# Kernel tuning notes

Hardware: AMD Instinct MI355X
Metric: run time of the kernel (lower is better)

## Reference

```python
import jax, jax.numpy as jnp
import numpy as np

EPS = 1e-12


def setup_inputs() -> dict:
    key = jax.random.key(0)
    k1, k2, k3, k4 = jax.random.split(key, 4)
    N, H, W, D, K = 64, 32, 32, 512, 64
    x = jax.random.normal(k1, (N, H, W, D), dtype=jnp.float32)
    W_assign = jax.random.normal(k2, (D, K), dtype=jnp.float32) * 0.05  # 1x1 conv kernel
    b_assign = jax.random.normal(k3, (K,), dtype=jnp.float32) * 0.05
    C = jax.random.normal(k4, (D, K), dtype=jnp.float32) * 0.05  # cluster centers
    return {"x": x, "W_assign": W_assign, "b_assign": b_assign, "C": C}


def _l2norm(v, axis):
    return v / jnp.sqrt(jnp.sum(v * v, axis=axis, keepdims=True) + EPS)


def reference(x, W_assign, b_assign, C):
    # 1x1 conv = matmul over channel dim: [N,H,W,D] @ [D,K] -> [N,H,W,K]
    s = jnp.einsum('nhwd,dk->nhwk', x, W_assign) + b_assign
    a = jax.nn.softmax(s, axis=-1)                       # soft assignment over K
    # VLAD: v[n,d,k] = sum_hw a[n,h,w,k] * (x[n,h,w,d] + C[d,k])
    # reformulated as two small contractions (no [N,H,W,D,K] intermediate):
    v = jnp.einsum('nhwd,nhwk->ndk', x, a)               # feature-weighted sums
    a_sum = jnp.sum(a, axis=(1, 2))                      # [N,K]
    v = v + a_sum[:, None, :] * C[None, :, :]            # [N,D,K]
    # intra-normalization: L2 over D per cluster (after transpose to [N,K,D])
    v = _l2norm(jnp.transpose(v, (0, 2, 1)), axis=-1)    # [N,K,D]
    v = jnp.transpose(v, (0, 2, 1))                      # [N,D,K]
    # flatten and final L2 normalize -> [N, D*K]
    v = v.reshape(v.shape[0], -1)
    return _l2norm(v, axis=-1)
```

## Files before the change

### kernel.cpp

```cpp
#include <hip/hip_runtime.h>


#define EPSF 1e-12f

typedef short bf16x8 __attribute__((ext_vector_type(8)));
typedef float f32x16 __attribute__((ext_vector_type(16)));

__device__ inline unsigned short f2bf_rne(float f) {
  union { float f; unsigned u; } v; v.f = f;
  unsigned u = v.u;
  unsigned r = u + 0x7fffu + ((u >> 16) & 1u);
  return (unsigned short)(r >> 16);
}
__device__ inline unsigned pk2(float a, float b) {
#if __has_builtin(__builtin_amdgcn_cvt_pk_bf16_f32)
  auto r = __builtin_amdgcn_cvt_pk_bf16_f32(a, b);
  return __builtin_bit_cast(unsigned, r);
#else
  return (unsigned)f2bf_rne(a) | ((unsigned)f2bf_rne(b) << 16);
#endif
}

__global__ __launch_bounds__(256) void kprep(
    const float* __restrict__ Wm, unsigned short* __restrict__ wt,
    float* __restrict__ stats ) {
  const int t = threadIdx.x, bx = blockIdx.x;
  if (bx == 8) {
    float4 z = {0.f, 0.f, 0.f, 0.f};
#pragma unroll
    for (int r = 0; r < 8; ++r)
      *(float4*)&stats[(size_t)(r * 256 + t) * 4] = z;
    return;
  }
  __shared__ float tile[64][65];
  {
    int col = (t & 15) * 4, rbase = t >> 4;
#pragma unroll
    for (int r = 0; r < 4; ++r) {
      int row = rbase + 16 * r;
      *(float4*)&tile[row][col] =
          *(const float4*)&Wm[(size_t)(bx * 64 + row) * 64 + col];
    }
  }
  __syncthreads();
  int k = t >> 2, seg = (t & 3) * 16;
  size_t o = (size_t)k * 512 + bx * 64 + seg;
#pragma unroll
  for (int j = 0; j < 16; j += 2)
    *(unsigned*)&wt[o + j] = pk2(tile[seg + j][k], tile[seg + j + 1][k]);
}

__global__ __launch_bounds__(256, 1) void kfused(
    const float* __restrict__ x, const unsigned short* __restrict__ wt,
    const float* __restrict__ b, float* __restrict__ vpart,
    float* __restrict__ a_sum) {
  __shared__ unsigned short xbT[512 * 128];
  __shared__ unsigned short ab[64 * 128];
  const int t = threadIdx.x;
  const int w = t >> 6, lane = t & 63, l31 = lane & 31, h = lane >> 5;
  const int bid = blockIdx.x;
  const int n = bid >> 2, c = bid & 3;
  const unsigned short* w0 = wt + (size_t)l31 * 512;
  const unsigned short* w1 = wt + (size_t)(32 + l31) * 512;
  const int colpx = w * 32 + l31;

  float bias0[16], bias1[16];
#pragma unroll
  for (int r = 0; r < 16; ++r) {
    const int k0 = (r & 3) + 8 * (r >> 2) + 4 * h;
    bias0[r] = b[k0];
    bias1[r] = b[k0 + 32];
  }

  f32x16 accv[8];
#pragma unroll
  for (int i = 0; i < 8; ++i)
#pragma unroll
    for (int j = 0; j < 16; ++j) accv[i][j] = 0.f;

  float sa0[16], sa1[16];
#pragma unroll
  for (int r = 0; r < 16; ++r) { sa0[r] = 0.f; sa1[r] = 0.f; }

  for (int s = 0; s < 2; ++s) {
    const int pxb = c * 256 + s * 128;
    const float* rowp = x + ((size_t)n * 1024 + pxb + colpx) * 512;
    f32x16 s0, s1;
#pragma unroll
    for (int i = 0; i < 16; ++i) { s0[i] = 0.f; s1[i] = 0.f; }
#pragma unroll 8
    for (int st = 0; st < 32; ++st) {
      const int kd = st * 16 + h * 8;
      float4 xa = *(const float4*)&rowp[kd];
      float4 xb = *(const float4*)&rowp[kd + 4];
      union { unsigned u[4]; bf16x8 v; } ax;
      ax.u[0] = pk2(xa.x, xa.y);
      ax.u[1] = pk2(xa.z, xa.w);
      ax.u[2] = pk2(xb.x, xb.y);
      ax.u[3] = pk2(xb.z, xb.w);
      bf16x8 b0 = *(const bf16x8*)&w0[kd];
      bf16x8 b1 = *(const bf16x8*)&w1[kd];
      s0 = __builtin_amdgcn_mfma_f32_32x32x16_bf16(b0, ax.v, s0, 0, 0, 0);
      s1 = __builtin_amdgcn_mfma_f32_32x32x16_bf16(b1, ax.v, s1, 0, 0, 0);
#pragma unroll
      for (int j2 = 0; j2 < 4; ++j2) {
        const int da = kd + 2 * j2, db = da + 1;
        xbT[da * 128 + (colpx ^ ((da & 15) << 3))] =
            (unsigned short)(ax.u[j2] & 0xffffu);
        xbT[db * 128 + (colpx ^ ((db & 15) << 3))] =
            (unsigned short)(ax.u[j2] >> 16);
      }
    }
    float v0[16], v1[16];
    float m = -3.402823466e+38f;
#pragma unroll
    for (int r = 0; r < 16; ++r) {
      v0[r] = s0[r] + bias0[r];
      v1[r] = s1[r] + bias1[r];
      m = fmaxf(m, fmaxf(v0[r], v1[r]));
    }
    m = fmaxf(m, __shfl_xor(m, 32, 64));
    float e0[16], e1[16];
    float S = 0.f;
#pragma unroll
    for (int r = 0; r < 16; ++r) {
      e0[r] = __expf(v0[r] - m);
      e1[r] = __expf(v1[r] - m);
      S += e0[r] + e1[r];
    }
    S += __shfl_xor(S, 32, 64);
    const float inv = 1.0f / S;
#pragma unroll
    for (int r = 0; r < 16; ++r) {
      const float a0 = e0[r] * inv, a1 = e1[r] * inv;
      sa0[r] += a0; sa1[r] += a1;
      const int k0 = (r & 3) + 8 * (r >> 2) + 4 * h, k1 = k0 + 32;
      ab[k0 * 128 + (colpx ^ ((k0 & 15) << 3))] = f2bf_rne(a0);
      ab[k1 * 128 + (colpx ^ ((k1 & 15) << 3))] = f2bf_rne(a1);
    }
    __syncthreads();
    const int dw = w * 128;
#pragma unroll
    for (int s8 = 0; s8 < 8; ++s8) {
      const int px0 = s8 * 16 + 8 * h;
      bf16x8 bb0 = *(const bf16x8*)&ab[l31 * 128 + (px0 ^ ((l31 & 15) << 3))];
      bf16x8 bb1 =
          *(const bf16x8*)&ab[(32 + l31) * 128 + (px0 ^ ((l31 & 15) << 3))];
#pragma unroll
      for (int dt = 0; dt < 4; ++dt) {
        const int dr = dw + dt * 32 + l31;
        bf16x8 aa = *(const bf16x8*)&xbT[dr * 128 + (px0 ^ ((dr & 15) << 3))];
        accv[dt * 2 + 0] =
            __builtin_amdgcn_mfma_f32_32x32x16_bf16(aa, bb0, accv[dt * 2 + 0], 0, 0, 0);
        accv[dt * 2 + 1] =
            __builtin_amdgcn_mfma_f32_32x32x16_bf16(aa, bb1, accv[dt * 2 + 1], 0, 0, 0);
      }
    }
    __syncthreads();
  }
#pragma unroll
  for (int msk = 1; msk < 32; msk <<= 1) {
#pragma unroll
    for (int r = 0; r < 16; ++r) {
      sa0[r] += __shfl_xor(sa0[r], msk, 64);
      sa1[r] += __shfl_xor(sa1[r], msk, 64);
    }
  }
  if (l31 < 16) {
    const int r = l31;
    const int k0 = (r & 3) + 8 * (r >> 2) + 4 * h;
    atomicAdd(&a_sum[n * 64 + k0], sa0[r]);
    atomicAdd(&a_sum[n * 64 + k0 + 32], sa1[r]);
  }
  float* vp = vpart + (size_t)c * 2097152 + (size_t)n * 32768;
#pragma unroll
  for (int dt = 0; dt < 4; ++dt) {
#pragma unroll
    for (int kt = 0; kt < 2; ++kt) {
      const f32x16 a = accv[dt * 2 + kt];
      const int kcol = kt * 32 + l31;
#pragma unroll
      for (int r = 0; r < 16; ++r) {
        const int drow = w * 128 + dt * 32 + (r & 3) + 8 * (r >> 2) + 4 * h;
        vp[drow * 64 + kcol] = a[r];
      }
    }
  }
}

__global__ __launch_bounds__(256) void kpost(
    const float* __restrict__ vpart, const float* __restrict__ a_sum,
    const float* __restrict__ C, float* __restrict__ out,
    float* __restrict__ ssq) {
  const int bid = blockIdx.x;
  const int n = bid & 63, d0 = (bid >> 6) * 64;
  const int t = threadIdx.x, k = t & 63, dr = t >> 6;
  const float as = a_sum[n * 64 + k];
  const size_t nb = (size_t)n * 32768;
  float sq = 0.f;
#pragma unroll
  for (int r = 0; r < 16; ++r) {
    const int d = d0 + dr * 16 + r;
    const size_t idx = nb + (size_t)d * 64 + k;
    float o = vpart[idx] + vpart[idx + 2097152] + vpart[idx + 4194304] +
              vpart[idx + 6291456] + as * C[(size_t)d * 64 + k];
    out[idx] = o;
    sq += o * o;
  }
  atomicAdd(&ssq[n * 64 + k], sq);
}

__global__ __launch_bounds__(256) void kscale(
    float* __restrict__ out, const float* __restrict__ ssq) {
  const int n = blockIdx.y, slice = blockIdx.x;
  const int t = threadIdx.x, k = t & 63, rg = t >> 6;
  __shared__ float sk[64];
  __shared__ float tot;
  if (t < 64) {
    float cc = ssq[n * 64 + t];
    sk[t] = rsqrtf(cc + EPSF);
    float contrib = cc / (cc + EPSF);
#pragma unroll
    for (int m = 32; m; m >>= 1) contrib += __shfl_xor(contrib, m, 64);
    if (t == 0) tot = rsqrtf(contrib + EPSF);
  }
  __syncthreads();
  const float scale = sk[k] * tot;
  float* vb = out + (size_t)n * 32768 + (size_t)slice * 4096;
#pragma unroll
  for (int r = rg; r < 64; r += 4) vb[r * 64 + k] *= scale;
}

extern "C" void kernel_launch(void* const* d_in, const int* in_sizes, int n_in,
                              void* d_out, int out_size, void* d_ws, size_t ws_size,
                              hipStream_t stream) {
  const float* x  = (const float*)d_in[0];
  const float* Wm = (const float*)d_in[1];
  const float* b  = (const float*)d_in[2];
  const float* C  = (const float*)d_in[3];
  float* out = (float*)d_out;

  float* vpart = (float*)d_ws;
  unsigned short* wt = (unsigned short*)(vpart + (size_t)4 * 2097152);
  float* stats = (float*)(wt + (size_t)64 * 512);
  float* a_sum = stats;
  float* ssq   = stats + 4096;

  kprep<<<dim3(9), dim3(256), 0, stream>>>(Wm, wt, stats);
  kfused<<<dim3(256), dim3(256), 0, stream>>>(x, wt, b, vpart, a_sum);
  kpost<<<dim3(512), dim3(256), 0, stream>>>(vpart, a_sum, C, out, ssq);
  kscale<<<dim3(8, 64), dim3(256), 0, stream>>>(out, ssq);
}
```

Before: 230.1 us.

## Drop LDS x-transpose, re-read x from global, split pixels over 8 blocks

The fused kernel no longer stages a 128 KB bf16 transpose of x in shared memory. Instead the second contraction re-reads x from global memory (likely L2-resident) with strided per-pixel loads and packs it to bf16 in registers. Each block now handles 128 pixels instead of 256, doubling the grid to 512 blocks and allowing more than one block per CU. The cost is a second read of x, strided uncoalesced-ish loads, and twice as many partial VLAD buffers for the post kernel to sum.

```diff
diff --git a/kernel.cpp b/kernel.cpp
--- a/kernel.cpp
+++ b/kernel.cpp
@@ -50,41 +50,21 @@
     *(unsigned*)&wt[o + j] = pk2(tile[seg + j][k], tile[seg + j + 1][k]);
 }
 
-__global__ __launch_bounds__(256, 1) void kfused(
+__global__ __launch_bounds__(256) void kfused(
     const float* __restrict__ x, const unsigned short* __restrict__ wt,
     const float* __restrict__ b, float* __restrict__ vpart,
     float* __restrict__ a_sum) {
-  __shared__ unsigned short xbT[512 * 128];
   __shared__ unsigned short ab[64 * 128];
   const int t = threadIdx.x;
   const int w = t >> 6, lane = t & 63, l31 = lane & 31, h = lane >> 5;
   const int bid = blockIdx.x;
-  const int n = bid >> 2, c = bid & 3;
+  const int n = bid >> 3, c = bid & 7;
   const unsigned short* w0 = wt + (size_t)l31 * 512;
   const unsigned short* w1 = wt + (size_t)(32 + l31) * 512;
   const int colpx = w * 32 + l31;
 
-  float bias0[16], bias1[16];
-#pragma unroll
-  for (int r = 0; r < 16; ++r) {
-    const int k0 = (r & 3) + 8 * (r >> 2) + 4 * h;
-    bias0[r] = b[k0];
-    bias1[r] = b[k0 + 32];
-  }
-
-  f32x16 accv[8];
-#pragma unroll
-  for (int i = 0; i < 8; ++i)
-#pragma unroll
-    for (int j = 0; j < 16; ++j) accv[i][j] = 0.f;
-
-  float sa0[16], sa1[16];
-#pragma unroll
-  for (int r = 0; r < 16; ++r) { sa0[r] = 0.f; sa1[r] = 0.f; }
-
-  for (int s = 0; s < 2; ++s) {
-    const int pxb = c * 256 + s * 128;
-    const float* rowp = x + ((size_t)n * 1024 + pxb + colpx) * 512;
+  {
+    const float* rowp = x + ((size_t)n * 1024 + c * 128 + colpx) * 512;
     f32x16 s0, s1;
 #pragma unroll
     for (int i = 0; i < 16; ++i) { s0[i] = 0.f; s1[i] = 0.f; }
@@ -102,76 +82,84 @@
       bf16x8 b1 = *(const bf16x8*)&w1[kd];
       s0 = __builtin_amdgcn_mfma_f32_32x32x16_bf16(b0, ax.v, s0, 0, 0, 0);
       s1 = __builtin_amdgcn_mfma_f32_32x32x16_bf16(b1, ax.v, s1, 0, 0, 0);
-#pragma unroll
-      for (int j2 = 0; j2 < 4; ++j2) {
-        const int da = kd + 2 * j2, db = da + 1;
-        xbT[da * 128 + (colpx ^ ((da & 15) << 3))] =
-            (unsigned short)(ax.u[j2] & 0xffffu);
-        xbT[db * 128 + (colpx ^ ((db & 15) << 3))] =
-            (unsigned short)(ax.u[j2] >> 16);
-      }
     }
     float v0[16], v1[16];
     float m = -3.402823466e+38f;
 #pragma unroll
     for (int r = 0; r < 16; ++r) {
-      v0[r] = s0[r] + bias0[r];
-      v1[r] = s1[r] + bias1[r];
+      const int k0 = (r & 3) + 8 * (r >> 2) + 4 * h;
+      v0[r] = s0[r] + b[k0];
+      v1[r] = s1[r] + b[k0 + 32];
       m = fmaxf(m, fmaxf(v0[r], v1[r]));
     }
     m = fmaxf(m, __shfl_xor(m, 32, 64));
-    float e0[16], e1[16];
+    float a0[16], a1[16];
     float S = 0.f;
 #pragma unroll
     for (int r = 0; r < 16; ++r) {
-      e0[r] = __expf(v0[r] - m);
-      e1[r] = __expf(v1[r] - m);
-      S += e0[r] + e1[r];
+      a0[r] = __expf(v0[r] - m);
+      a1[r] = __expf(v1[r] - m);
+      S += a0[r] + a1[r];
     }
     S += __shfl_xor(S, 32, 64);
     const float inv = 1.0f / S;
 #pragma unroll
     for (int r = 0; r < 16; ++r) {
-      const float a0 = e0[r] * inv, a1 = e1[r] * inv;
-      sa0[r] += a0; sa1[r] += a1;
+      a0[r] *= inv; a1[r] *= inv;
       const int k0 = (r & 3) + 8 * (r >> 2) + 4 * h, k1 = k0 + 32;
-      ab[k0 * 128 + (colpx ^ ((k0 & 15) << 3))] = f2bf_rne(a0);
-      ab[k1 * 128 + (colpx ^ ((k1 & 15) << 3))] = f2bf_rne(a1);
-    }
-    __syncthreads();
-    const int dw = w * 128;
-#pragma unroll
-    for (int s8 = 0; s8 < 8; ++s8) {
-      const int px0 = s8 * 16 + 8 * h;
-      bf16x8 bb0 = *(const bf16x8*)&ab[l31 * 128 + (px0 ^ ((l31 & 15) << 3))];
-      bf16x8 bb1 =
-          *(const bf16x8*)&ab[(32 + l31) * 128 + (px0 ^ ((l31 & 15) << 3))];
-#pragma unroll
-      for (int dt = 0; dt < 4; ++dt) {
-        const int dr = dw + dt * 32 + l31;
-        bf16x8 aa = *(const bf16x8*)&xbT[dr * 128 + (px0 ^ ((dr & 15) << 3))];
-        accv[dt * 2 + 0] =
-            __builtin_amdgcn_mfma_f32_32x32x16_bf16(aa, bb0, accv[dt * 2 + 0], 0, 0, 0);
-        accv[dt * 2 + 1] =
-            __builtin_amdgcn_mfma_f32_32x32x16_bf16(aa, bb1, accv[dt * 2 + 1], 0, 0, 0);
+      ab[k0 * 128 + (colpx ^ ((k0 & 15) << 3))] = f2bf_rne(a0[r]);
+      ab[k1 * 128 + (colpx ^ ((k1 & 15) << 3))] = f2bf_rne(a1[r]);
+    }
+#pragma unroll
+    for (int msk = 1; msk < 32; msk <<= 1) {
+#pragma unroll
+      for (int r = 0; r < 16; ++r) {
+        a0[r] += __shfl_xor(a0[r], msk, 64);
+        a1[r] += __shfl_xor(a1[r], msk, 64);
       }
     }
-    __syncthreads();
-  }
-#pragma unroll
-  for (int msk = 1; msk < 32; msk <<= 1) {
-#pragma unroll
-    for (int r = 0; r < 16; ++r) {
-      sa0[r] += __shfl_xor(sa0[r], msk, 64);
-      sa1[r] += __shfl_xor(sa1[r], msk, 64);
-    }
-  }
-  if (l31 < 16) {
-    const int r = l31;
-    const int k0 = (r & 3) + 8 * (r >> 2) + 4 * h;
-    atomicAdd(&a_sum[n * 64 + k0], sa0[r]);
-    atomicAdd(&a_sum[n * 64 + k0 + 32], sa1[r]);
-  }
+    if (l31 < 16) {
+      const int r = l31;
+      const int k0 = (r & 3) + 8 * (r >> 2) + 4 * h;
+      atomicAdd(&a_sum[n * 64 + k0], a0[r]);
+      atomicAdd(&a_sum[n * 64 + k0 + 32], a1[r]);
+    }
+  }
+  __syncthreads();
+
+  const int dw = w * 128;
+  f32x16 accv[8];
+#pragma unroll
+  for (int i = 0; i < 8; ++i)
+#pragma unroll
+    for (int j = 0; j < 16; ++j) accv[i][j] = 0.f;
+
+  const float* xg = x + ((size_t)n * 1024 + c * 128) * 512;
+#pragma unroll 2
+  for (int m = 0; m < 8; ++m) {
+    const int px0 = m * 16 + h * 8;
+    bf16x8 bb0 = *(const bf16x8*)&ab[l31 * 128 + (px0 ^ ((l31 & 15) << 3))];
+    bf16x8 bb1 =
+        *(const bf16x8*)&ab[(32 + l31) * 128 + (px0 ^ ((l31 & 15) << 3))];
+#pragma unroll
+    for (int dt = 0; dt < 4; ++dt) {
+      const int d = dw + dt * 32 + l31;
+      const float* xp = xg + (size_t)px0 * 512 + d;
+      float a[8];
+#pragma unroll
+      for (int j = 0; j < 8; ++j) a[j] = xp[(size_t)j * 512];
+      union { unsigned u[4]; bf16x8 v; } aa;
+      aa.u[0] = pk2(a[0], a[1]);
+      aa.u[1] = pk2(a[2], a[3]);
+      aa.u[2] = pk2(a[4], a[5]);
+      aa.u[3] = pk2(a[6], a[7]);
+      accv[dt * 2 + 0] =
+          __builtin_amdgcn_mfma_f32_32x32x16_bf16(aa.v, bb0, accv[dt * 2 + 0], 0, 0, 0);
+      accv[dt * 2 + 1] =
+          __builtin_amdgcn_mfma_f32_32x32x16_bf16(aa.v, bb1, accv[dt * 2 + 1], 0, 0, 0);
+    }
+  }
+
   float* vp = vpart + (size_t)c * 2097152 + (size_t)n * 32768;
 #pragma unroll
   for (int dt = 0; dt < 4; ++dt) {
@@ -181,7 +169,7 @@
       const int kcol = kt * 32 + l31;
 #pragma unroll
       for (int r = 0; r < 16; ++r) {
-        const int drow = w * 128 + dt * 32 + (r & 3) + 8 * (r >> 2) + 4 * h;
+        const int drow = dw + dt * 32 + (r & 3) + 8 * (r >> 2) + 4 * h;
         vp[drow * 64 + kcol] = a[r];
       }
     }
@@ -202,8 +190,9 @@
   for (int r = 0; r < 16; ++r) {
     const int d = d0 + dr * 16 + r;
     const size_t idx = nb + (size_t)d * 64 + k;
-    float o = vpart[idx] + vpart[idx + 2097152] + vpart[idx + 4194304] +
-              vpart[idx + 6291456] + as * C[(size_t)d * 64 + k];
+    float o = as * C[(size_t)d * 64 + k];
+#pragma unroll
+    for (int cc = 0; cc < 8; ++cc) o += vpart[idx + (size_t)cc * 2097152];
     out[idx] = o;
     sq += o * o;
   }
@@ -241,13 +230,13 @@
   float* out = (float*)d_out;
 
   float* vpart = (float*)d_ws;
-  unsigned short* wt = (unsigned short*)(vpart + (size_t)4 * 2097152);
+  unsigned short* wt = (unsigned short*)(vpart + (size_t)8 * 2097152);
   float* stats = (float*)(wt + (size_t)64 * 512);
   float* a_sum = stats;
   float* ssq   = stats + 4096;
 
   kprep<<<dim3(9), dim3(256), 0, stream>>>(Wm, wt, stats);
-  kfused<<<dim3(256), dim3(256), 0, stream>>>(x, wt, b, vpart, a_sum);
+  kfused<<<dim3(512), dim3(256), 0, stream>>>(x, wt, b, vpart, a_sum);
   kpost<<<dim3(512), dim3(256), 0, stream>>>(vpart, a_sum, C, out, ssq);
   kscale<<<dim3(8, 64), dim3(256), 0, stream>>>(out, ssq);
 }
```

New measurement: 254.2 us. 10.5% more time.

## Double-buffer LDS tiles and overlap VLAD MFMA with next chunk's loads

Applied to the files above, without the earlier changes.

Shrinks the per-step pixel chunk from 128 to 64 and splits the channel dimension of the assignment GEMM across wave pairs, reducing partial logits through LDS scratch. LDS tiles for x and assignments are double-buffered so the VLAD accumulation MFMAs for the previous chunk are interleaved with global loads and conversion of the current chunk. This aims to hide global memory latency behind matrix work. It adds extra syncs and an LDS reduction step, and reuses the previous buffer as scratch. Softmax now runs on half the waves.

```diff
diff --git a/kernel.cpp b/kernel.cpp
--- a/kernel.cpp
+++ b/kernel.cpp
@@ -54,123 +54,158 @@
     const float* __restrict__ x, const unsigned short* __restrict__ wt,
     const float* __restrict__ b, float* __restrict__ vpart,
     float* __restrict__ a_sum) {
-  __shared__ unsigned short xbT[512 * 128];
-  __shared__ unsigned short ab[64 * 128];
+  __shared__ unsigned short xbT[2][512 * 64];
+  __shared__ unsigned short ab[2][64 * 64];
   const int t = threadIdx.x;
   const int w = t >> 6, lane = t & 63, l31 = lane & 31, h = lane >> 5;
   const int bid = blockIdx.x;
   const int n = bid >> 2, c = bid & 3;
-  const unsigned short* w0 = wt + (size_t)l31 * 512;
-  const unsigned short* w1 = wt + (size_t)(32 + l31) * 512;
-  const int colpx = w * 32 + l31;
-
-  float bias0[16], bias1[16];
-#pragma unroll
-  for (int r = 0; r < 16; ++r) {
-    const int k0 = (r & 3) + 8 * (r >> 2) + 4 * h;
-    bias0[r] = b[k0];
-    bias1[r] = b[k0 + 32];
-  }
+  const int pxl = (w >> 1) * 32 + l31;
+  const int dhalf = (w & 1) * 256;
+  const unsigned short* wk0 = wt + (size_t)l31 * 512;
+  const unsigned short* wk1 = wt + (size_t)(32 + l31) * 512;
 
   f32x16 accv[8];
 #pragma unroll
   for (int i = 0; i < 8; ++i)
 #pragma unroll
     for (int j = 0; j < 16; ++j) accv[i][j] = 0.f;
-
   float sa0[16], sa1[16];
 #pragma unroll
   for (int r = 0; r < 16; ++r) { sa0[r] = 0.f; sa1[r] = 0.f; }
 
-  for (int s = 0; s < 2; ++s) {
-    const int pxb = c * 256 + s * 128;
-    const float* rowp = x + ((size_t)n * 1024 + pxb + colpx) * 512;
+#pragma unroll
+  for (int s = 0; s < 4; ++s) {
+    const int cur = s & 1, prv = (s + 1) & 1;
+    const float* rowp =
+        x + ((size_t)n * 1024 + c * 256 + s * 64 + pxl) * 512 + dhalf;
     f32x16 s0, s1;
 #pragma unroll
     for (int i = 0; i < 16; ++i) { s0[i] = 0.f; s1[i] = 0.f; }
-#pragma unroll 8
-    for (int st = 0; st < 32; ++st) {
-      const int kd = st * 16 + h * 8;
-      float4 xa = *(const float4*)&rowp[kd];
-      float4 xb = *(const float4*)&rowp[kd + 4];
-      union { unsigned u[4]; bf16x8 v; } ax;
-      ax.u[0] = pk2(xa.x, xa.y);
-      ax.u[1] = pk2(xa.z, xa.w);
-      ax.u[2] = pk2(xb.x, xb.y);
-      ax.u[3] = pk2(xb.z, xb.w);
-      bf16x8 b0 = *(const bf16x8*)&w0[kd];
-      bf16x8 b1 = *(const bf16x8*)&w1[kd];
-      s0 = __builtin_amdgcn_mfma_f32_32x32x16_bf16(b0, ax.v, s0, 0, 0, 0);
-      s1 = __builtin_amdgcn_mfma_f32_32x32x16_bf16(b1, ax.v, s1, 0, 0, 0);
-#pragma unroll
-      for (int j2 = 0; j2 < 4; ++j2) {
-        const int da = kd + 2 * j2, db = da + 1;
-        xbT[da * 128 + (colpx ^ ((da & 15) << 3))] =
-            (unsigned short)(ax.u[j2] & 0xffffu);
-        xbT[db * 128 + (colpx ^ ((db & 15) << 3))] =
-            (unsigned short)(ax.u[j2] >> 16);
-      }
-    }
-    float v0[16], v1[16];
-    float m = -3.402823466e+38f;
-#pragma unroll
-    for (int r = 0; r < 16; ++r) {
-      v0[r] = s0[r] + bias0[r];
-      v1[r] = s1[r] + bias1[r];
-      m = fmaxf(m, fmaxf(v0[r], v1[r]));
-    }
-    m = fmaxf(m, __shfl_xor(m, 32, 64));
-    float e0[16], e1[16];
-    float S = 0.f;
-#pragma unroll
-    for (int r = 0; r < 16; ++r) {
-      e0[r] = __expf(v0[r] - m);
-      e1[r] = __expf(v1[r] - m);
-      S += e0[r] + e1[r];
-    }
-    S += __shfl_xor(S, 32, 64);
-    const float inv = 1.0f / S;
-#pragma unroll
-    for (int r = 0; r < 16; ++r) {
-      const float a0 = e0[r] * inv, a1 = e1[r] * inv;
-      sa0[r] += a0; sa1[r] += a1;
-      const int k0 = (r & 3) + 8 * (r >> 2) + 4 * h, k1 = k0 + 32;
-      ab[k0 * 128 + (colpx ^ ((k0 & 15) << 3))] = f2bf_rne(a0);
-      ab[k1 * 128 + (colpx ^ ((k1 & 15) << 3))] = f2bf_rne(a1);
+
+#pragma unroll
+    for (int u = 0; u < 2; ++u) {
+      float4 xs[16];
+#pragma unroll
+      for (int j = 0; j < 8; ++j) {
+        const int kd = (u * 8 + j) * 16 + h * 8;
+        xs[2 * j]     = *(const float4*)&rowp[kd];
+        xs[2 * j + 1] = *(const float4*)&rowp[kd + 4];
+      }
+      if (s > 0) {
+#pragma unroll
+        for (int ks = 2 * u; ks < 2 * u + 2; ++ks) {
+          const int px0 = ks * 16 + h * 8;
+          bf16x8 bb0 =
+              *(const bf16x8*)&ab[prv][l31 * 64 + (px0 ^ ((l31 & 7) << 3))];
+          bf16x8 bb1 = *(const bf16x8*)&ab[prv][(32 + l31) * 64 +
+                                               (px0 ^ ((l31 & 7) << 3))];
+#pragma unroll
+          for (int dt = 0; dt < 4; ++dt) {
+            const int dr = 128 * w + dt * 32 + l31;
+            bf16x8 aa =
+                *(const bf16x8*)&xbT[prv][dr * 64 + (px0 ^ ((dr & 7) << 3))];
+            accv[dt * 2 + 0] = __builtin_amdgcn_mfma_f32_32x32x16_bf16(
+                aa, bb0, accv[dt * 2 + 0], 0, 0, 0);
+            accv[dt * 2 + 1] = __builtin_amdgcn_mfma_f32_32x32x16_bf16(
+                aa, bb1, accv[dt * 2 + 1], 0, 0, 0);
+          }
+        }
+      }
+#pragma unroll
+      for (int j = 0; j < 8; ++j) {
+        const int kd = (u * 8 + j) * 16 + h * 8;
+        union { unsigned uu[4]; bf16x8 v; } ax;
+        ax.uu[0] = pk2(xs[2 * j].x, xs[2 * j].y);
+        ax.uu[1] = pk2(xs[2 * j].z, xs[2 * j].w);
+        ax.uu[2] = pk2(xs[2 * j + 1].x, xs[2 * j + 1].y);
+        ax.uu[3] = pk2(xs[2 * j + 1].z, xs[2 * j + 1].w);
+#pragma unroll
+        for (int j2 = 0; j2 < 4; ++j2) {
+          const int da = dhalf + kd + 2 * j2, db = da + 1;
+          xbT[cur][da * 64 + (pxl ^ ((da & 7) << 3))] =
+              (unsigned short)(ax.uu[j2] & 0xffffu);
+          xbT[cur][db * 64 + (pxl ^ ((db & 7) << 3))] =
+              (unsigned short)(ax.uu[j2] >> 16);
+        }
+        bf16x8 b0 = *(const bf16x8*)&wk0[dhalf + kd];
+        bf16x8 b1 = *(const bf16x8*)&wk1[dhalf + kd];
+        s0 = __builtin_amdgcn_mfma_f32_32x32x16_bf16(b0, ax.v, s0, 0, 0, 0);
+        s1 = __builtin_amdgcn_mfma_f32_32x32x16_bf16(b1, ax.v, s1, 0, 0, 0);
+      }
     }
     __syncthreads();
-    const int dw = w * 128;
-#pragma unroll
-    for (int s8 = 0; s8 < 8; ++s8) {
-      const int px0 = s8 * 16 + 8 * h;
-      bf16x8 bb0 = *(const bf16x8*)&ab[l31 * 128 + (px0 ^ ((l31 & 15) << 3))];
-      bf16x8 bb1 =
-          *(const bf16x8*)&ab[(32 + l31) * 128 + (px0 ^ ((l31 & 15) << 3))];
-#pragma unroll
-      for (int dt = 0; dt < 4; ++dt) {
-        const int dr = dw + dt * 32 + l31;
-        bf16x8 aa = *(const bf16x8*)&xbT[dr * 128 + (px0 ^ ((dr & 15) << 3))];
-        accv[dt * 2 + 0] =
-            __builtin_amdgcn_mfma_f32_32x32x16_bf16(aa, bb0, accv[dt * 2 + 0], 0, 0, 0);
-        accv[dt * 2 + 1] =
-            __builtin_amdgcn_mfma_f32_32x32x16_bf16(aa, bb1, accv[dt * 2 + 1], 0, 0, 0);
-      }
+    float* scr = (float*)&xbT[prv][0];
+    if ((w & 1) == 0) {
+      float* my = scr + (w >> 1) * 4096 + lane * 32;
+#pragma unroll
+      for (int r = 0; r < 16; ++r) { my[r] = s0[r]; my[16 + r] = s1[r]; }
     }
     __syncthreads();
-  }
-#pragma unroll
-  for (int msk = 1; msk < 32; msk <<= 1) {
-#pragma unroll
-    for (int r = 0; r < 16; ++r) {
-      sa0[r] += __shfl_xor(sa0[r], msk, 64);
-      sa1[r] += __shfl_xor(sa1[r], msk, 64);
-    }
-  }
-  if (l31 < 16) {
-    const int r = l31;
-    const int k0 = (r & 3) + 8 * (r >> 2) + 4 * h;
-    atomicAdd(&a_sum[n * 64 + k0], sa0[r]);
-    atomicAdd(&a_sum[n * 64 + k0 + 32], sa1[r]);
+    if (w & 1) {
+      const float* my = scr + (w >> 1) * 4096 + lane * 32;
+      float v0[16], v1[16];
+      float m = -3.402823466e+38f;
+#pragma unroll
+      for (int r = 0; r < 16; ++r) {
+        const int k0 = (r & 3) + 8 * (r >> 2) + 4 * h;
+        v0[r] = s0[r] + my[r] + b[k0];
+        v1[r] = s1[r] + my[16 + r] + b[k0 + 32];
+        m = fmaxf(m, fmaxf(v0[r], v1[r]));
+      }
+      m = fmaxf(m, __shfl_xor(m, 32, 64));
+      float a0[16], a1[16];
+      float S = 0.f;
+#pragma unroll
+      for (int r = 0; r < 16; ++r) {
+        a0[r] = __expf(v0[r] - m);
+        a1[r] = __expf(v1[r] - m);
+        S += a0[r] + a1[r];
+      }
+      S += __shfl_xor(S, 32, 64);
+      const float inv = 1.0f / S;
+#pragma unroll
+      for (int r = 0; r < 16; ++r) {
+        a0[r] *= inv; a1[r] *= inv;
+        sa0[r] += a0[r]; sa1[r] += a1[r];
+        const int k0 = (r & 3) + 8 * (r >> 2) + 4 * h, k1 = k0 + 32;
+        ab[cur][k0 * 64 + (pxl ^ ((k0 & 7) << 3))] = f2bf_rne(a0[r]);
+        ab[cur][k1 * 64 + (pxl ^ ((k1 & 7) << 3))] = f2bf_rne(a1[r]);
+      }
+    }
+    __syncthreads();
+  }
+#pragma unroll
+  for (int ks = 0; ks < 4; ++ks) {
+    const int px0 = ks * 16 + h * 8;
+    bf16x8 bb0 = *(const bf16x8*)&ab[1][l31 * 64 + (px0 ^ ((l31 & 7) << 3))];
+    bf16x8 bb1 =
+        *(const bf16x8*)&ab[1][(32 + l31) * 64 + (px0 ^ ((l31 & 7) << 3))];
+#pragma unroll
+    for (int dt = 0; dt < 4; ++dt) {
+      const int dr = 128 * w + dt * 32 + l31;
+      bf16x8 aa = *(const bf16x8*)&xbT[1][dr * 64 + (px0 ^ ((dr & 7) << 3))];
+      accv[dt * 2 + 0] = __builtin_amdgcn_mfma_f32_32x32x16_bf16(
+          aa, bb0, accv[dt * 2 + 0], 0, 0, 0);
+      accv[dt * 2 + 1] = __builtin_amdgcn_mfma_f32_32x32x16_bf16(
+          aa, bb1, accv[dt * 2 + 1], 0, 0, 0);
+    }
+  }
+  if (w & 1) {
+#pragma unroll
+    for (int msk = 1; msk < 32; msk <<= 1) {
+#pragma unroll
+      for (int r = 0; r < 16; ++r) {
+        sa0[r] += __shfl_xor(sa0[r], msk, 64);
+        sa1[r] += __shfl_xor(sa1[r], msk, 64);
+      }
+    }
+    if (l31 < 16) {
+      const int r = l31;
+      const int k0 = (r & 3) + 8 * (r >> 2) + 4 * h;
+      atomicAdd(&a_sum[n * 64 + k0], sa0[r]);
+      atomicAdd(&a_sum[n * 64 + k0 + 32], sa1[r]);
+    }
   }
   float* vp = vpart + (size_t)c * 2097152 + (size_t)n * 32768;
 #pragma unroll
@@ -181,7 +216,7 @@
       const int kcol = kt * 32 + l31;
 #pragma unroll
       for (int r = 0; r < 16; ++r) {
-        const int drow = w * 128 + dt * 32 + (r & 3) + 8 * (r >> 2) + 4 * h;
+        const int drow = 128 * w + dt * 32 + (r & 3) + 8 * (r >> 2) + 4 * h;
         vp[drow * 64 + kcol] = a[r];
       }
     }
@@ -202,8 +237,9 @@
   for (int r = 0; r < 16; ++r) {
     const int d = d0 + dr * 16 + r;
     const size_t idx = nb + (size_t)d * 64 + k;
-    float o = vpart[idx] + vpart[idx + 2097152] + vpart[idx + 4194304] +
-              vpart[idx + 6291456] + as * C[(size_t)d * 64 + k];
+    float o = as * C[(size_t)d * 64 + k];
+#pragma unroll
+    for (int cc = 0; cc < 4; ++cc) o += vpart[idx + (size_t)cc * 2097152];
     out[idx] = o;
     sq += o * o;
   }
```

Measured after the change: 258.3 us. +12.2%, slower.
